# Performance work log

Measured on AMD Instinct MI355X. Metric: run time of the kernel, lower is better.

## Reference

```python
import jax, jax.numpy as jnp
import numpy as np

NUM_HEADS = 16


def setup_inputs() -> dict:
    key = jax.random.key(0)
    ks = jax.random.split(key, 10)
    B, C, T, K, E = 2, 4, 512, 1024, 1024
    s = 0.02
    return {
        "hidden_states": jax.random.normal(ks[0], (B, T, E), jnp.float32),
        "key_value_states": jax.random.normal(ks[1], (B, C, K, E), jnp.float32),
        "Wq": jax.random.normal(ks[2], (E, E), jnp.float32) * s,
        "bq": jax.random.normal(ks[3], (E,), jnp.float32) * s,
        "Wk": jax.random.normal(ks[4], (E, E), jnp.float32) * s,
        "bk": jax.random.normal(ks[5], (E,), jnp.float32) * s,
        "Wv": jax.random.normal(ks[6], (E, E), jnp.float32) * s,
        "bv": jax.random.normal(ks[7], (E,), jnp.float32) * s,
        "Wo": jax.random.normal(ks[8], (E, E), jnp.float32) * s,
        "bo": jax.random.normal(ks[9], (E,), jnp.float32) * s,
    }


def reference(hidden_states, key_value_states, Wq, bq, Wk, bk, Wv, bv, Wo, bo):
    B, C, K, E = key_value_states.shape
    T = hidden_states.shape[1]
    H = NUM_HEADS
    Dh = E // H
    scaling = Dh ** (-0.5)
    # q: [B,H,T,Dh]
    q = ((hidden_states @ Wq.T + bq) * scaling).reshape(B, T, H, Dh).transpose(0, 2, 1, 3)
    # k, v: [B,H,K,C,Dh]  (matches torch view(B,C,K,H,Dh).transpose(1,3))
    k = (key_value_states @ Wk.T + bk).reshape(B, C, K, H, Dh).transpose(0, 3, 2, 1, 4)
    v = (key_value_states @ Wv.T + bv).reshape(B, C, K, H, Dh).transpose(0, 3, 2, 1, 4)
    # scores: [B,H,T,K,C]; softmax over kv_len axis (per channel)
    scores = jnp.einsum("bhtd,bhkcd->bhtkc", q, k)
    probs = jax.nn.softmax(scores, axis=3)
    # default channel pooling weight = 1/C (channel_weight=None path)
    cw = jnp.full((B, C), 1.0 / C, dtype=probs.dtype)
    # attend + weighted channel-sum -> [B,T,H,Dh] -> [B,T,E]
    attn = jnp.einsum("bhtkc,bhkcd,bc->bthd", probs, v, cw).reshape(B, T, E)
    return attn @ Wo.T + bo
```

## Files before the change

kernel.cpp:

```cpp
#include <hip/hip_runtime.h>
#include <hip/hip_bf16.h>

#define DIM_B 2
#define DIM_C 4
#define DIM_T 512
#define DIM_K 1024
#define DIM_E 1024
#define DIM_H 16
#define DIM_DH 64

typedef __attribute__((ext_vector_type(8))) short bf16x8;
typedef __attribute__((ext_vector_type(4))) short bf16x4;
typedef __attribute__((ext_vector_type(4))) float f32x4;
typedef __attribute__((ext_vector_type(2))) unsigned int u32x2;

#define MFMA_BF16(a, b, c) __builtin_amdgcn_mfma_f32_16x16x32_bf16((a), (b), (c), 0, 0, 0)

static __device__ __forceinline__ short f2bf(float f) {
    union { float f; unsigned u; } v; v.f = f;
    unsigned r = v.u + 0x7fffu + ((v.u >> 16) & 1u);
    return (short)(r >> 16);
}

static __device__ __forceinline__ unsigned pack_bf2(float lo, float hi) {
    union { float f; unsigned u; } a, b; a.f = lo; b.f = hi;
    return (a.u >> 16) | (b.u & 0xffff0000u);
}

static __device__ __forceinline__ void gload16(const short* g, short* lds) {
    __builtin_amdgcn_global_load_lds(
        (const __attribute__((address_space(1))) unsigned int*)g,
        (__attribute__((address_space(3))) unsigned int*)lds, 16, 0, 0);
}

__global__ __launch_bounds__(256) void cast6(
    const float* __restrict__ kvs, const float* __restrict__ hs,
    const float* __restrict__ wq, const float* __restrict__ wk,
    const float* __restrict__ wv, const float* __restrict__ wo,
    short* kvsb, short* hsb, short* wqb, short* wkb, short* wvb, short* wob)
{
    int blk = blockIdx.x;
    const float* src; short* dst; size_t off;
    if (blk < 4096) { src = kvs; dst = kvsb; off = (size_t)blk * 2048; }
    else {
        int s = (blk - 4096) >> 9;
        off = (size_t)((blk - 4096) & 511) * 2048;
        switch (s) {
            case 0: src = hs; dst = hsb; break;
            case 1: src = wq; dst = wqb; break;
            case 2: src = wk; dst = wkb; break;
            case 3: src = wv; dst = wvb; break;
            default: src = wo; dst = wob; break;
        }
    }
    size_t i = off + (size_t)threadIdx.x * 8;
    float4 a = *(const float4*)(src + i);
    float4 b = *(const float4*)(src + i + 4);
    bf16x8 o;
    o[0] = f2bf(a.x); o[1] = f2bf(a.y); o[2] = f2bf(a.z); o[3] = f2bf(a.w);
    o[4] = f2bf(b.x); o[5] = f2bf(b.y); o[6] = f2bf(b.z); o[7] = f2bf(b.w);
    *(bf16x8*)(dst + i) = o;
}

template <bool A_BF16, bool OUT_BF16, bool BIAS_ROW>
static __device__ __forceinline__ void gemm_tile(
    const void* __restrict__ Av, const short* __restrict__ W,
    const float* __restrict__ bias, void* __restrict__ Ov,
    int N, int Kd, float scale, int bm, int bn, short* As, short* Bs)
{
    const int tid = threadIdx.x;
    const int wave = tid >> 6, lane = tid & 63;
    const int L = lane & 15, Q = lane >> 4;
    const int wm = (wave & 1) * 64, wn = (wave >> 1) * 64;
    const int lr = lane >> 3;
    const int lc = ((lane & 7) ^ lr) * 8;

    f32x4 acc[4][4] = {};

    for (int k0 = 0; k0 < Kd; k0 += 64) {
        __syncthreads();
        if (A_BF16) {
            const short* A = (const short*)Av;
#pragma unroll
            for (int i = 0; i < 4; ++i) {
                int r = wave * 32 + i * 8;
                gload16(A + (size_t)(bm + r + lr) * Kd + k0 + lc, As + r * 64);
            }
        } else {
            const float* A = (const float*)Av;
#pragma unroll
            for (int rep = 0; rep < 4; ++rep) {
                int row = (tid >> 3) + rep * 32;
                int p = tid & 7;
                const float* src = A + (size_t)(bm + row) * Kd + k0 + p * 8;
                float4 a = *(const float4*)src;
                float4 b = *(const float4*)(src + 4);
                bf16x8 o;
                o[0] = f2bf(a.x); o[1] = f2bf(a.y); o[2] = f2bf(a.z); o[3] = f2bf(a.w);
                o[4] = f2bf(b.x); o[5] = f2bf(b.y); o[6] = f2bf(b.z); o[7] = f2bf(b.w);
                *(bf16x8*)&As[row * 64 + ((p ^ (row & 7)) * 8)] = o;
            }
        }
#pragma unroll
        for (int i = 0; i < 4; ++i) {
            int r = wave * 32 + i * 8;
            gload16(W + (size_t)(bn + r + lr) * Kd + k0 + lc, Bs + r * 64);
        }
        __syncthreads();
#pragma unroll
        for (int s = 0; s < 2; ++s) {
            bf16x8 af[4], bfr[4];
#pragma unroll
            for (int i = 0; i < 4; ++i)
                af[i] = *(const bf16x8*)&As[(wm + i * 16 + L) * 64 + (((s * 4 + Q) ^ (L & 7)) * 8)];
#pragma unroll
            for (int j = 0; j < 4; ++j)
                bfr[j] = *(const bf16x8*)&Bs[(wn + j * 16 + L) * 64 + (((s * 4 + Q) ^ (L & 7)) * 8)];
#pragma unroll
            for (int i = 0; i < 4; ++i)
#pragma unroll
                for (int j = 0; j < 4; ++j)
                    acc[i][j] = MFMA_BF16(af[i], bfr[j], acc[i][j]);
        }
    }

#pragma unroll
    for (int i = 0; i < 4; ++i) {
        int row0 = bm + wm + i * 16 + Q * 4;
#pragma unroll
        for (int j = 0; j < 4; ++j) {
            int col = bn + wn + j * 16 + L;
            float bj = BIAS_ROW ? 0.f : bias[col];
#pragma unroll
            for (int r = 0; r < 4; ++r) {
                float bb = BIAS_ROW ? bias[row0 + r] : bj;
                float o = (acc[i][j][r] + bb) * scale;
                if (OUT_BF16)
                    ((short*)Ov)[(size_t)(row0 + r) * N + col] = f2bf(o);
                else
                    ((float*)Ov)[(size_t)(row0 + r) * N + col] = o;
            }
        }
    }
}

template <bool A_BF16, bool OUT_BF16, int A_SUM>
static __device__ __forceinline__ void gemm_tile64(
    const void* __restrict__ Av, const short* __restrict__ W,
    const float* __restrict__ bias, void* __restrict__ Ov,
    int N, int Kd, float scale, int bm, int bn, short* As, short* Bs)
{
    const int tid = threadIdx.x;
    const int wave = tid >> 6, lane = tid & 63;
    const int L = lane & 15, Q = lane >> 4;
    const int wm = (wave & 1) * 32, wn = (wave >> 1) * 32;
    const int lr = lane >> 3;
    const int lc = ((lane & 7) ^ lr) * 8;

    f32x4 acc[2][2] = {};

    for (int k0 = 0; k0 < Kd; k0 += 64) {
        __syncthreads();
        if (A_BF16) {
            const short* A = (const short*)Av;
#pragma unroll
            for (int i = 0; i < 2; ++i) {
                int r = wave * 16 + i * 8;
                gload16(A + (size_t)(bm + r + lr) * Kd + k0 + lc, As + r * 64);
            }
        } else {
            const float* A = (const float*)Av;
#pragma unroll
            for (int rep = 0; rep < 2; ++rep) {
                int row = (tid >> 3) + rep * 32;
                int p = tid & 7;
                size_t base = (size_t)(bm + row) * Kd + k0 + p * 8;
                float va[8] = {0.f, 0.f, 0.f, 0.f, 0.f, 0.f, 0.f, 0.f};
#pragma unroll
                for (int cc = 0; cc < A_SUM; ++cc) {
                    const float* src = A + (size_t)cc * (1u << 20) + base;
                    float4 a = *(const float4*)src;
                    float4 b = *(const float4*)(src + 4);
                    va[0] += a.x; va[1] += a.y; va[2] += a.z; va[3] += a.w;
                    va[4] += b.x; va[5] += b.y; va[6] += b.z; va[7] += b.w;
                }
                bf16x8 o;
#pragma unroll
                for (int e = 0; e < 8; ++e) o[e] = f2bf(va[e]);
                *(bf16x8*)&As[row * 64 + ((p ^ (row & 7)) * 8)] = o;
            }
        }
#pragma unroll
        for (int i = 0; i < 2; ++i) {
            int r = wave * 16 + i * 8;
            gload16(W + (size_t)(bn + r + lr) * Kd + k0 + lc, Bs + r * 64);
        }
        __syncthreads();
#pragma unroll
        for (int s = 0; s < 2; ++s) {
            bf16x8 af[2], bfr[2];
#pragma unroll
            for (int i = 0; i < 2; ++i)
                af[i] = *(const bf16x8*)&As[(wm + i * 16 + L) * 64 + (((s * 4 + Q) ^ (L & 7)) * 8)];
#pragma unroll
            for (int j = 0; j < 2; ++j)
                bfr[j] = *(const bf16x8*)&Bs[(wn + j * 16 + L) * 64 + (((s * 4 + Q) ^ (L & 7)) * 8)];
#pragma unroll
            for (int i = 0; i < 2; ++i)
#pragma unroll
                for (int j = 0; j < 2; ++j)
                    acc[i][j] = MFMA_BF16(af[i], bfr[j], acc[i][j]);
        }
    }

#pragma unroll
    for (int i = 0; i < 2; ++i) {
        int row0 = bm + wm + i * 16 + Q * 4;
#pragma unroll
        for (int j = 0; j < 2; ++j) {
            int col = bn + wn + j * 16 + L;
            float bj = bias[col];
#pragma unroll
            for (int r = 0; r < 4; ++r) {
                float o = (acc[i][j][r] + bj) * scale;
                if (OUT_BF16)
                    ((short*)Ov)[(size_t)(row0 + r) * N + col] = f2bf(o);
                else
                    ((float*)Ov)[(size_t)(row0 + r) * N + col] = o;
            }
        }
    }
}

__global__ __launch_bounds__(256) void gemm_qkv(
    const short* __restrict__ hsb, const short* __restrict__ wqb,
    const float* __restrict__ bq, short* __restrict__ qb,
    const short* __restrict__ kvsb, const short* __restrict__ wkb,
    const float* __restrict__ bk, short* __restrict__ kb,
    const short* __restrict__ wvb, const float* __restrict__ bv,
    short* __restrict__ vtb)
{
    __shared__ alignas(16) short As[128 * 64];
    __shared__ alignas(16) short Bs[128 * 64];
    int blk = blockIdx.x;
    if (blk < 256) {
        int i = blk;
        int bm = (i & 7) + 8 * (i >> 7);
        int bn = (i >> 3) & 15;
        gemm_tile64<true, true, 1>(hsb, wqb, bq, qb, DIM_E, DIM_E, 0.125f,
                                   bm * 64, bn * 64, As, Bs);
    } else if (blk < 768) {
        int i = blk - 256;
        int bm = (i & 7) + 8 * (i >> 6);
        int bn = (i >> 3) & 7;
        gemm_tile<true, true, false>(kvsb, wkb, bk, kb, DIM_E, DIM_E, 1.0f,
                                     bm * 128, bn * 128, As, Bs);
    } else {
        int i = blk - 768;
        int bn = (i & 7) + 8 * (i >> 6);
        int bm = (i >> 3) & 7;
        gemm_tile<true, true, true>(wvb, kvsb, bv, vtb, DIM_B * DIM_C * DIM_K, DIM_E, 1.0f,
                                    bm * 128, bn * 128, As, Bs);
    }
}

__global__ __launch_bounds__(256) void gemm_o(
    const float* __restrict__ A, const short* __restrict__ W,
    const float* __restrict__ bias, float* __restrict__ Out)
{
    __shared__ alignas(16) short As[64 * 64];
    __shared__ alignas(16) short Bs[64 * 64];
    int i = blockIdx.x;
    int bm = (i & 7) + 8 * (i >> 7);
    int bn = (i >> 3) & 15;
    gemm_tile64<false, false, 4>(A, W, bias, Out, DIM_E, DIM_E, 1.0f,
                                 bm * 64, bn * 64, As, Bs);
}

__global__ __launch_bounds__(512) void attn_kernel(
    const short* __restrict__ q, const short* __restrict__ k,
    const short* __restrict__ vt, float* __restrict__ abc)
{
    __shared__ alignas(16) short Ks[64 * 64];
    __shared__ alignas(16) short Vs[64 * 64];
    __shared__ alignas(16) short Pl[8][16][72];

    const int tid = threadIdx.x;
    const int wave = tid >> 6, lane = tid & 63;
    const int L = lane & 15, Q = lane >> 4;
    const int lr = lane >> 3;
    const int lc = ((lane & 7) ^ lr) * 8;
    const int x = blockIdx.x;
    const int low = x & 7;
    const int c = low & 3, b = low >> 2;
    const int y = x >> 3;
    const int tt = y & 3, h = y >> 2;
    const int t0 = tt * 128;
    const int NKV = DIM_B * DIM_C * DIM_K;

    const size_t qrow = (size_t)(b * DIM_T + t0 + wave * 16 + L) * DIM_E + h * DIM_DH;
    const bf16x8 aq0 = *(const bf16x8*)(q + qrow + Q * 8);
    const bf16x8 aq1 = *(const bf16x8*)(q + qrow + 32 + Q * 8);

    const size_t kbase = (size_t)((b * DIM_C + c) * DIM_K) * DIM_E + h * DIM_DH;
    const size_t vbase = (size_t)(h * DIM_DH) * NKV + (b * DIM_C + c) * DIM_K;

    float lsum = 0.f;
    f32x4 oacc[4] = {};

    const int xs0 = (Q ^ (L & 7)) * 8;
    const int xs1 = ((4 + Q) ^ (L & 7)) * 8;

    for (int kc = 0; kc < 16; ++kc) {
        const int kk0 = kc * 64;
        __syncthreads();
        {
            int r = wave * 8;
            gload16(k + kbase + (size_t)(kk0 + r + lr) * DIM_E + lc, Ks + r * 64);
            gload16(vt + vbase + (size_t)(r + lr) * NKV + kk0 + lc, Vs + r * 64);
        }
        __syncthreads();
        f32x4 s4[4];
#pragma unroll
        for (int j = 0; j < 4; ++j) {
            bf16x8 bk0 = *(const bf16x8*)&Ks[(j * 16 + L) * 64 + xs0];
            bf16x8 bk1 = *(const bf16x8*)&Ks[(j * 16 + L) * 64 + xs1];
            f32x4 z = {};
            z = MFMA_BF16(bk0, aq0, z);
            s4[j] = MFMA_BF16(bk1, aq1, z);
        }
#pragma unroll
        for (int j = 0; j < 4; ++j) {
            float p0 = __expf(s4[j][0]), p1 = __expf(s4[j][1]);
            float p2 = __expf(s4[j][2]), p3 = __expf(s4[j][3]);
            lsum += (p0 + p1) + (p2 + p3);
            u32x2 w;
            w[0] = pack_bf2(p0, p1);
            w[1] = pack_bf2(p2, p3);
            *(u32x2*)&Pl[wave][L][j * 16 + Q * 4] = w;
        }
        bf16x8 ap0 = *(const bf16x8*)&Pl[wave][L][Q * 8];
        bf16x8 ap1 = *(const bf16x8*)&Pl[wave][L][32 + Q * 8];
#pragma unroll
        for (int dt = 0; dt < 4; ++dt) {
            bf16x8 bv0 = *(const bf16x8*)&Vs[(dt * 16 + L) * 64 + xs0];
            bf16x8 bv1 = *(const bf16x8*)&Vs[(dt * 16 + L) * 64 + xs1];
            oacc[dt] = MFMA_BF16(ap0, bv0, oacc[dt]);
            oacc[dt] = MFMA_BF16(ap1, bv1, oacc[dt]);
        }
    }

    float lr_ = lsum;
    lr_ += __shfl_xor(lr_, 16);
    lr_ += __shfl_xor(lr_, 32);
    float linv[4];
#pragma unroll
    for (int r = 0; r < 4; ++r)
        linv[r] = 0.25f / __shfl(lr_, Q * 4 + r);

    float* dst = abc + ((size_t)c << 20);
#pragma unroll
    for (int dt = 0; dt < 4; ++dt)
#pragma unroll
        for (int r = 0; r < 4; ++r) {
            int t = t0 + wave * 16 + Q * 4 + r;
            int d = dt * 16 + L;
            dst[(size_t)(b * DIM_T + t) * DIM_E + h * DIM_DH + d] = oacc[dt][r] * linv[r];
        }
}

extern "C" void kernel_launch(void* const* d_in, const int* in_sizes, int n_in,
                              void* d_out, int out_size, void* d_ws, size_t ws_size,
                              hipStream_t stream)
{
    const float* hs  = (const float*)d_in[0];
    const float* kvs = (const float*)d_in[1];
    const float* Wq  = (const float*)d_in[2];
    const float* bq  = (const float*)d_in[3];
    const float* Wk  = (const float*)d_in[4];
    const float* bk  = (const float*)d_in[5];
    const float* Wv  = (const float*)d_in[6];
    const float* bv  = (const float*)d_in[7];
    const float* Wo  = (const float*)d_in[8];
    const float* bo  = (const float*)d_in[9];
    float* out = (float*)d_out;

    char* ws = (char*)d_ws;
    short* kvsb = (short*)(ws);
    short* hsb  = (short*)(ws + (16ull << 20));
    short* wqb  = (short*)(ws + (18ull << 20));
    short* wkb  = (short*)(ws + (20ull << 20));
    short* wvb  = (short*)(ws + (22ull << 20));
    short* wob  = (short*)(ws + (24ull << 20));
    short* qb   = (short*)(ws + (26ull << 20));
    short* kb   = (short*)(ws + (28ull << 20));
    short* vtb  = (short*)(ws + (44ull << 20));
    float* abc  = (float*)(ws);

    dim3 blk(256);

    cast6<<<dim3(4096 + 5 * 512), blk, 0, stream>>>(
        kvs, hs, Wq, Wk, Wv, Wo, kvsb, hsb, wqb, wkb, wvb, wob);

    gemm_qkv<<<dim3(256 + 512 + 512), blk, 0, stream>>>(
        hsb, wqb, bq, qb, kvsb, wkb, bk, kb, wvb, bv, vtb);

    attn_kernel<<<dim3(512), dim3(512), 0, stream>>>(qb, kb, vtb, abc);

    gemm_o<<<dim3(256), blk, 0, stream>>>(abc, wob, bo, out);
}
```

Measured before the change: 211.3 us.

## Fuse K and V projection GEMMs into one tile sharing the key/value input

The separate K and V projection tiles are replaced by one kernel tile that loads the key/value-states slab once into shared memory and multiplies it against both Wk and Wv. K is produced row-major and V transposed, from two accumulator sets. This halves the reads of the large bf16 key/value input and the block count for that stage. In exchange each block holds 32 accumulator vectors and 48 KB of LDS, which raises register pressure and may cut occupancy; launch bounds now request 2 blocks per SM.

Result: faster. 200.2 us (-5.3%).

```diff
diff --git a/kernel.cpp b/kernel.cpp
--- a/kernel.cpp
+++ b/kernel.cpp
@@ -62,84 +62,75 @@
     *(bf16x8*)(dst + i) = o;
 }
 
-template <bool A_BF16, bool OUT_BF16, bool BIAS_ROW>
-static __device__ __forceinline__ void gemm_tile(
-    const void* __restrict__ Av, const short* __restrict__ W,
-    const float* __restrict__ bias, void* __restrict__ Ov,
-    int N, int Kd, float scale, int bm, int bn, short* As, short* Bs)
+static __device__ __forceinline__ void gemm_tile_kv(
+    const short* __restrict__ kv, const short* __restrict__ wk,
+    const short* __restrict__ wv, const float* __restrict__ bk,
+    const float* __restrict__ bv, short* __restrict__ kout,
+    short* __restrict__ vtout, int bm, int bn,
+    short* As, short* Bs, short* Cs)
 {
     const int tid = threadIdx.x;
     const int wave = tid >> 6, lane = tid & 63;
     const int L = lane & 15, Q = lane >> 4;
-    const int wm = (wave & 1) * 64, wn = (wave >> 1) * 64;
+    const int wmK = (wave & 1) * 64, wnK = (wave >> 1) * 64;
     const int lr = lane >> 3;
     const int lc = ((lane & 7) ^ lr) * 8;
 
-    f32x4 acc[4][4] = {};
-
-    for (int k0 = 0; k0 < Kd; k0 += 64) {
-        __syncthreads();
-        if (A_BF16) {
-            const short* A = (const short*)Av;
-#pragma unroll
-            for (int i = 0; i < 4; ++i) {
-                int r = wave * 32 + i * 8;
-                gload16(A + (size_t)(bm + r + lr) * Kd + k0 + lc, As + r * 64);
-            }
-        } else {
-            const float* A = (const float*)Av;
-#pragma unroll
-            for (int rep = 0; rep < 4; ++rep) {
-                int row = (tid >> 3) + rep * 32;
-                int p = tid & 7;
-                const float* src = A + (size_t)(bm + row) * Kd + k0 + p * 8;
-                float4 a = *(const float4*)src;
-                float4 b = *(const float4*)(src + 4);
-                bf16x8 o;
-                o[0] = f2bf(a.x); o[1] = f2bf(a.y); o[2] = f2bf(a.z); o[3] = f2bf(a.w);
-                o[4] = f2bf(b.x); o[5] = f2bf(b.y); o[6] = f2bf(b.z); o[7] = f2bf(b.w);
-                *(bf16x8*)&As[row * 64 + ((p ^ (row & 7)) * 8)] = o;
-            }
-        }
+    f32x4 accK[4][4] = {};
+    f32x4 accV[4][4] = {};
+
+    for (int k0 = 0; k0 < DIM_E; k0 += 64) {
+        __syncthreads();
 #pragma unroll
         for (int i = 0; i < 4; ++i) {
             int r = wave * 32 + i * 8;
-            gload16(W + (size_t)(bn + r + lr) * Kd + k0 + lc, Bs + r * 64);
+            gload16(kv + (size_t)(bm + r + lr) * DIM_E + k0 + lc, As + r * 64);
+            gload16(wk + (size_t)(bn + r + lr) * DIM_E + k0 + lc, Bs + r * 64);
+            gload16(wv + (size_t)(bn + r + lr) * DIM_E + k0 + lc, Cs + r * 64);
         }
         __syncthreads();
 #pragma unroll
         for (int s = 0; s < 2; ++s) {
-            bf16x8 af[4], bfr[4];
+            bf16x8 fkv[4], fwk[4], fwv[4];
+            const int xo = ((s * 4 + Q) ^ (L & 7)) * 8;
+#pragma unroll
+            for (int i = 0; i < 4; ++i) {
+                fkv[i] = *(const bf16x8*)&As[(wmK + i * 16 + L) * 64 + xo];
+                fwk[i] = *(const bf16x8*)&Bs[(wnK + i * 16 + L) * 64 + xo];
+                fwv[i] = *(const bf16x8*)&Cs[(wnK + i * 16 + L) * 64 + xo];
+            }
 #pragma unroll
             for (int i = 0; i < 4; ++i)
-                af[i] = *(const bf16x8*)&As[(wm + i * 16 + L) * 64 + (((s * 4 + Q) ^ (L & 7)) * 8)];
-#pragma unroll
-            for (int j = 0; j < 4; ++j)
-                bfr[j] = *(const bf16x8*)&Bs[(wn + j * 16 + L) * 64 + (((s * 4 + Q) ^ (L & 7)) * 8)];
-#pragma unroll
-            for (int i = 0; i < 4; ++i)
-#pragma unroll
-                for (int j = 0; j < 4; ++j)
-                    acc[i][j] = MFMA_BF16(af[i], bfr[j], acc[i][j]);
+#pragma unroll
+                for (int j = 0; j < 4; ++j) {
+                    accK[i][j] = MFMA_BF16(fkv[i], fwk[j], accK[i][j]);
+                    accV[i][j] = MFMA_BF16(fwv[i], fkv[j], accV[i][j]);
+                }
         }
     }
 
 #pragma unroll
     for (int i = 0; i < 4; ++i) {
-        int row0 = bm + wm + i * 16 + Q * 4;
+        int row0 = bm + wmK + i * 16 + Q * 4;
 #pragma unroll
         for (int j = 0; j < 4; ++j) {
-            int col = bn + wn + j * 16 + L;
-            float bj = BIAS_ROW ? 0.f : bias[col];
-#pragma unroll
-            for (int r = 0; r < 4; ++r) {
-                float bb = BIAS_ROW ? bias[row0 + r] : bj;
-                float o = (acc[i][j][r] + bb) * scale;
-                if (OUT_BF16)
-                    ((short*)Ov)[(size_t)(row0 + r) * N + col] = f2bf(o);
-                else
-                    ((float*)Ov)[(size_t)(row0 + r) * N + col] = o;
-            }
+            int col = bn + wnK + j * 16 + L;
+            float bb = bk[col];
+#pragma unroll
+            for (int r = 0; r < 4; ++r)
+                kout[(size_t)(row0 + r) * DIM_E + col] = f2bf(accK[i][j][r] + bb);
+        }
+    }
+#pragma unroll
+    for (int i = 0; i < 4; ++i) {
+        int row0 = bn + wnK + i * 16 + Q * 4;
+#pragma unroll
+        for (int j = 0; j < 4; ++j) {
+            int col = bm + wmK + j * 16 + L;
+#pragma unroll
+            for (int r = 0; r < 4; ++r)
+                vtout[(size_t)(row0 + r) * (DIM_B * DIM_C * DIM_K) + col] =
+                    f2bf(accV[i][j][r] + bv[row0 + r]);
         }
     }
 }
@@ -232,7 +223,7 @@
     }
 }
 
-__global__ __launch_bounds__(256) void gemm_qkv(
+__global__ __launch_bounds__(256, 2) void gemm_qkv(
     const short* __restrict__ hsb, const short* __restrict__ wqb,
     const float* __restrict__ bq, short* __restrict__ qb,
     const short* __restrict__ kvsb, const short* __restrict__ wkb,
@@ -242,6 +233,7 @@
 {
     __shared__ alignas(16) short As[128 * 64];
     __shared__ alignas(16) short Bs[128 * 64];
+    __shared__ alignas(16) short Cs[128 * 64];
     int blk = blockIdx.x;
     if (blk < 256) {
         int i = blk;
@@ -249,18 +241,12 @@
         int bn = (i >> 3) & 15;
         gemm_tile64<true, true, 1>(hsb, wqb, bq, qb, DIM_E, DIM_E, 0.125f,
                                    bm * 64, bn * 64, As, Bs);
-    } else if (blk < 768) {
+    } else {
         int i = blk - 256;
         int bm = (i & 7) + 8 * (i >> 6);
         int bn = (i >> 3) & 7;
-        gemm_tile<true, true, false>(kvsb, wkb, bk, kb, DIM_E, DIM_E, 1.0f,
-                                     bm * 128, bn * 128, As, Bs);
-    } else {
-        int i = blk - 768;
-        int bn = (i & 7) + 8 * (i >> 6);
-        int bm = (i >> 3) & 7;
-        gemm_tile<true, true, true>(wvb, kvsb, bv, vtb, DIM_B * DIM_C * DIM_K, DIM_E, 1.0f,
-                                    bm * 128, bn * 128, As, Bs);
+        gemm_tile_kv(kvsb, wkb, wvb, bk, bv, kb, vtb,
+                     bm * 128, bn * 128, As, Bs, Cs);
     }
 }
 
@@ -402,7 +388,7 @@
     cast6<<<dim3(4096 + 5 * 512), blk, 0, stream>>>(
         kvs, hs, Wq, Wk, Wv, Wo, kvsb, hsb, wqb, wkb, wvb, wob);
 
-    gemm_qkv<<<dim3(256 + 512 + 512), blk, 0, stream>>>(
+    gemm_qkv<<<dim3(256 + 512), blk, 0, stream>>>(
         hsb, wqb, bq, qb, kvsb, wkb, bk, kb, wvb, bv, vtb);
 
     attn_kernel<<<dim3(512), dim3(512), 0, stream>>>(qb, kb, vtb, abc);
```
